# Performance work log

Measured on AMD Instinct MI355X. Metric: run time of the kernel, lower is better.

Reference implementation:

```python
import jax, jax.numpy as jnp
import numpy as np

EPS = 1e-5
DN = ('NCHW', 'OIHW', 'NCHW')


def _bn(x, g, b, m, v):
    # eval-mode batchnorm: per-channel affine with running stats
    scale = (g / jnp.sqrt(v + EPS))[None, :, None, None]
    return (x - m[None, :, None, None]) * scale + b[None, :, None, None]


def setup_inputs() -> dict:
    key = jax.random.key(0)
    ks = jax.random.split(key, 11)
    B, T, Cin, HID, H, W, K = 8, 20, 64, 64, 64, 64, 3
    CC = Cin + HID          # 128 channels into depthwise conv
    C4 = 4 * HID            # 256 gate channels
    return {
        'x': jax.random.normal(ks[0], (B, T, Cin, H, W), jnp.float32),
        'dw_w': jax.random.normal(ks[1], (CC, 1, K, K), jnp.float32) * 0.1,
        'gamma1': jax.random.uniform(ks[2], (CC,), jnp.float32, 0.5, 1.5),
        'beta1': jax.random.normal(ks[3], (CC,), jnp.float32) * 0.1,
        'mean1': jax.random.normal(ks[4], (CC,), jnp.float32) * 0.1,
        'var1': jax.random.uniform(ks[5], (CC,), jnp.float32, 0.5, 1.5),
        'pw_w': jax.random.normal(ks[6], (C4, CC, 1, 1), jnp.float32) * 0.05,
        'gamma2': jax.random.uniform(ks[7], (C4,), jnp.float32, 0.5, 1.5),
        'beta2': jax.random.normal(ks[8], (C4,), jnp.float32) * 0.1,
        'mean2': jax.random.normal(ks[9], (C4,), jnp.float32) * 0.1,
        'var2': jax.random.uniform(ks[10], (C4,), jnp.float32, 0.5, 1.5),
    }


def reference(x, dw_w, gamma1, beta1, mean1, var1, pw_w, gamma2, beta2, mean2, var2):
    B, T, Cin, H, W = x.shape
    hid = pw_w.shape[0] // 4
    cc = dw_w.shape[0]

    def cell(h, c, x_t):
        z = jnp.concatenate([x_t, h], axis=1)                 # (B, Cin+hid, H, W)
        z = jax.lax.conv_general_dilated(z, dw_w, (1, 1), 'SAME',
                                         dimension_numbers=DN,
                                         feature_group_count=cc)
        z = jax.nn.selu(_bn(z, gamma1, beta1, mean1, var1))
        z = jax.lax.conv_general_dilated(z, pw_w, (1, 1), 'SAME',
                                         dimension_numbers=DN)
        z = jax.nn.selu(_bn(z, gamma2, beta2, mean2, var2))   # (B, 4*hid, H, W)
        # NOTE: original code applies Sigmoid to all four gates (incl. g)
        i, f, o, g = jnp.split(jax.nn.sigmoid(z), 4, axis=1)
        c_next = f * c + i * g
        h_next = o * jnp.tanh(c_next)
        return h_next, c_next

    h0 = jnp.zeros((B, hid, H, W), x.dtype)
    c0 = jnp.zeros((B, hid, H, W), x.dtype)

    def step(carry, x_t):
        h, c = cell(carry[0], carry[1], x_t)
        return (h, c), h

    xs = jnp.moveaxis(x, 1, 0)                # (T, B, Cin, H, W)
    _, hs = jax.lax.scan(step, (h0, c0), xs)  # hs: (T, B, hid, H, W)
    return jnp.moveaxis(hs, 0, 1)             # (B, T, hid, H, W)
```

## Files before the change

kernel.cpp:

```cpp
#include <hip/hip_runtime.h>
#include <math.h>

typedef _Float16 half8 __attribute__((ext_vector_type(8)));
typedef float float4v __attribute__((ext_vector_type(4)));

#define SELU_ALPHA 1.6732632423543772f
#define SELU_SCALE 1.0507009873554805f

__device__ __forceinline__ float selu_f(float x) {
    return x > 0.f ? SELU_SCALE * x : SELU_SCALE * SELU_ALPHA * (__expf(x) - 1.f);
}
__device__ __forceinline__ float gate_f(float a, float sc, float sh) {
    float z = a * sc + sh;
    float s = selu_f(z);
    return 1.f / (1.f + __expf(-s));
}

__global__ __launch_bounds__(256) void prep_kernel(
    const float* __restrict__ pw_w,
    const float* __restrict__ g1, const float* __restrict__ b1,
    const float* __restrict__ m1, const float* __restrict__ v1,
    const float* __restrict__ g2, const float* __restrict__ b2,
    const float* __restrict__ m2, const float* __restrict__ v2,
    const float* __restrict__ dw_w,
    _Float16* __restrict__ wB, float* __restrict__ bn2, float* __restrict__ dwpk)
{
    int i = blockIdx.x * 256 + threadIdx.x;
    if (i < 32768) {
        wB[i] = (_Float16)pw_w[i];
    } else if (i < 32768 + 256) {
        int c = i - 32768;
        float sc = g2[c] * rsqrtf(v2[c] + 1e-5f);
        bn2[c] = sc;
        bn2[256 + c] = b2[c] - m2[c] * sc;
    } else if (i < 32768 + 256 + 1536) {
        int j = i - 33024;
        int c = j / 12, k = j - c * 12;
        float val;
        if (k < 9) {
            val = dw_w[c * 9 + k];
        } else {
            float sc = g1[c] * rsqrtf(v1[c] + 1e-5f);
            if (k == 9) val = sc;
            else if (k == 10) val = b1[c] - m1[c] * sc;
            else val = 0.f;
        }
        dwpk[c * 12 + k] = val;
    }
}

__global__ __launch_bounds__(256, 2) void cell_kernel(
    const float* __restrict__ x, const float* __restrict__ hsrc,
    const float* __restrict__ dwpk, const _Float16* __restrict__ wB,
    const float* __restrict__ bn2,
    float* __restrict__ cbuf, float* __restrict__ out, int t)
{
    __shared__ _Float16 Alds[64 * 136];

    int tid = threadIdx.x;
    int bid = blockIdx.y * 64 + blockIdx.x;
    int mapped = (bid & 7) * 64 + (bid >> 3);
    int y0 = mapped & 63;
    int b = mapped >> 6;
    int s0 = y0 << 6;

    int w = tid >> 6;
    int lane = tid & 63;
    int col = lane & 15, quad = lane >> 4;
    int hc = w * 16 + col;

    half8 bfr[4][4];
    #pragma unroll
    for (int nt = 0; nt < 4; ++nt)
        #pragma unroll
        for (int kc = 0; kc < 4; ++kc)
            bfr[nt][kc] = *(const half8*)(wB + (size_t)((nt << 6) + hc) * 128 + kc * 32 + quad * 8);

    bool hwave = (w >= 2);
    const float* src0;
    if (!hwave)
        src0 = x + (((size_t)(b * 20 + t) * 64 + (w << 5)) << 12);
    else
        src0 = hsrc + (((size_t)(b * 20 + (t - 1)) * 64 + ((w - 2) << 5)) << 12);

    if (hwave && t == 0) {
        #pragma unroll
        for (int it = 0; it < 16; ++it) {
            int cc = (w << 5) + (it << 1);
            float sha = dwpk[cc * 12 + 10];
            float shb = dwpk[cc * 12 + 22];
            Alds[lane * 136 + cc]     = (_Float16)selu_f(sha);
            Alds[lane * 136 + cc + 1] = (_Float16)selu_f(shb);
        }
    } else {
        #pragma unroll 4
        for (int it = 0; it < 16; ++it) {
            int cl = it << 1;
            int cc = (w << 5) + cl;
            const float* chA = src0 + ((size_t)cl << 12);
            const float* chB = chA + 4096;
            int p = s0 + lane;
            float a0 = (y0 > 0)  ? chA[p - 64] : 0.f;
            float a1 = chA[p];
            float a2 = (y0 < 63) ? chA[p + 64] : 0.f;
            float c0 = (y0 > 0)  ? chB[p - 64] : 0.f;
            float c1 = chB[p];
            float c2 = (y0 < 63) ? chB[p + 64] : 0.f;
            const float4v* wp = (const float4v*)(dwpk + cc * 12);
            float4v wa0 = wp[0], wa1 = wp[1], wa2 = wp[2];
            float4v wb0 = wp[3], wb1 = wp[4], wb2 = wp[5];
            float P  = fmaf(wa0[0], a0, fmaf(wa0[3], a1, wa1[2] * a2));
            float Q  = fmaf(wa0[1], a0, fmaf(wa1[0], a1, wa1[3] * a2));
            float R  = fmaf(wa0[2], a0, fmaf(wa1[1], a1, wa2[0] * a2));
            float P2 = fmaf(wb0[0], c0, fmaf(wb0[3], c1, wb1[2] * c2));
            float Q2 = fmaf(wb0[1], c0, fmaf(wb1[0], c1, wb1[3] * c2));
            float R2 = fmaf(wb0[2], c0, fmaf(wb1[1], c1, wb2[0] * c2));
            float Pl  = __shfl_up(P, 1);    if (lane == 0)  Pl  = 0.f;
            float Rr  = __shfl_down(R, 1);  if (lane == 63) Rr  = 0.f;
            float P2l = __shfl_up(P2, 1);   if (lane == 0)  P2l = 0.f;
            float R2r = __shfl_down(R2, 1); if (lane == 63) R2r = 0.f;
            float za = fmaf(Pl + Q + Rr,   wa2[1], wa2[2]);
            float zb = fmaf(P2l + Q2 + R2r, wb2[1], wb2[2]);
            Alds[lane * 136 + cc]     = (_Float16)selu_f(za);
            Alds[lane * 136 + cc + 1] = (_Float16)selu_f(zb);
        }
    }

    __syncthreads();

    float4v acc[4][4];
    #pragma unroll
    for (int mt = 0; mt < 4; ++mt)
        #pragma unroll
        for (int nt = 0; nt < 4; ++nt)
            acc[mt][nt] = (float4v){0.f, 0.f, 0.f, 0.f};

    #pragma unroll
    for (int kc = 0; kc < 4; ++kc) {
        half8 a[4];
        #pragma unroll
        for (int mt = 0; mt < 4; ++mt)
            a[mt] = *(const half8*)(Alds + (mt * 16 + col) * 136 + kc * 32 + quad * 8);
        #pragma unroll
        for (int mt = 0; mt < 4; ++mt)
            #pragma unroll
            for (int nt = 0; nt < 4; ++nt)
                acc[mt][nt] = __builtin_amdgcn_mfma_f32_16x16x32_f16(a[mt], bfr[nt][kc], acc[mt][nt], 0, 0, 0);
    }

    float sc[4], sh[4];
    #pragma unroll
    for (int nt = 0; nt < 4; ++nt) {
        sc[nt] = bn2[(nt << 6) + hc];
        sh[nt] = bn2[256 + (nt << 6) + hc];
    }

    size_t cbase = (((size_t)(b * 64 + hc)) << 12) + s0;
    size_t obase = (((size_t)((b * 20 + t) * 64 + hc)) << 12) + s0;

    #pragma unroll
    for (int mt = 0; mt < 4; ++mt) {
        #pragma unroll
        for (int r = 0; r < 4; ++r) {
            int sl = mt * 16 + quad * 4 + r;
            float gi = gate_f(acc[mt][0][r], sc[0], sh[0]);
            float gf = gate_f(acc[mt][1][r], sc[1], sh[1]);
            float go = gate_f(acc[mt][2][r], sc[2], sh[2]);
            float gg = gate_f(acc[mt][3][r], sc[3], sh[3]);
            float cp = (t == 0) ? 0.f : cbuf[cbase + sl];
            float cn = gf * cp + gi * gg;
            cbuf[cbase + sl] = cn;
            float th = 1.f - 2.f / (__expf(2.f * cn) + 1.f);
            out[obase + sl] = go * th;
        }
    }
}

extern "C" void kernel_launch(void* const* d_in, const int* in_sizes, int n_in,
                              void* d_out, int out_size, void* d_ws, size_t ws_size,
                              hipStream_t stream) {
    const float* x    = (const float*)d_in[0];
    const float* dw_w = (const float*)d_in[1];
    const float* g1   = (const float*)d_in[2];
    const float* b1   = (const float*)d_in[3];
    const float* m1   = (const float*)d_in[4];
    const float* v1   = (const float*)d_in[5];
    const float* g2   = (const float*)d_in[6];
    const float* b2   = (const float*)d_in[7];
    const float* m2   = (const float*)d_in[8];
    const float* v2   = (const float*)d_in[9];
    const float* pw_w = (const float*)d_in[6 - 2 + 2];
    (void)pw_w;
    const float* pw_w_ = (const float*)d_in[6];
    const float* g2_   = (const float*)d_in[7];
    const float* b2_   = (const float*)d_in[8];
    const float* m2_   = (const float*)d_in[9];
    const float* v2_   = (const float*)d_in[10];
    float* out = (float*)d_out;

    _Float16* wB16 = (_Float16*)d_ws;
    float* bn2  = (float*)d_ws + 16384;
    float* dwpk = bn2 + 512;
    float* cbuf = dwpk + 1536;

    prep_kernel<<<135, 256, 0, stream>>>(pw_w_, g1, b1, m1, v1,
                                         g2_, b2_, m2_, v2_, dw_w,
                                         wB16, bn2, dwpk);

    for (int t = 0; t < 20; ++t) {
        cell_kernel<<<dim3(64, 8), 256, 0, stream>>>(x, out, dwpk, wB16, bn2,
                                                     cbuf, out, t);
    }
}
```

Baseline: 836.2 us.

## Fuse all timesteps into one persistent kernel with neighbor-row flag sync

Replaces the 20 per-timestep launches with a single persistent kernel of 256 blocks. Each block owns two image rows of one batch element, keeps the cell state in registers instead of a global buffer, and waits on per-row flags set by the neighboring row blocks before reading the previous hidden state for the halo. This removes launch overhead and the global c-state traffic. In exchange it relies on all 256 blocks being co-resident to avoid deadlock, and it adds system-scope fences and spin-waits.

```diff
diff --git a/kernel.cpp b/kernel.cpp
--- a/kernel.cpp
+++ b/kernel.cpp
@@ -23,7 +23,8 @@
     const float* __restrict__ g2, const float* __restrict__ b2,
     const float* __restrict__ m2, const float* __restrict__ v2,
     const float* __restrict__ dw_w,
-    _Float16* __restrict__ wB, float* __restrict__ bn2, float* __restrict__ dwpk)
+    _Float16* __restrict__ wB, float* __restrict__ bn2, float* __restrict__ dwpk,
+    int* __restrict__ flags)
 {
     int i = blockIdx.x * 256 + threadIdx.x;
     if (i < 32768) {
@@ -46,28 +47,70 @@
             else val = 0.f;
         }
         dwpk[c * 12 + k] = val;
-    }
-}
-
-__global__ __launch_bounds__(256, 2) void cell_kernel(
-    const float* __restrict__ x, const float* __restrict__ hsrc,
-    const float* __restrict__ dwpk, const _Float16* __restrict__ wB,
-    const float* __restrict__ bn2,
-    float* __restrict__ cbuf, float* __restrict__ out, int t)
+    } else if (i < 32768 + 256 + 1536 + 256) {
+        flags[i - 34560] = 0;
+    }
+}
+
+__device__ __forceinline__ void dw_rows(
+    const float* __restrict__ src0, const float* __restrict__ dwpk,
+    int ccbase, int y0, int lane, _Float16* Alds)
 {
-    __shared__ _Float16 Alds[64 * 136];
+    int p = (y0 << 6) + lane;
+    #pragma unroll 4
+    for (int it = 0; it < 16; ++it) {
+        int cl = it << 1;
+        int cc = ccbase + cl;
+        const float* chA = src0 + ((size_t)cl << 12);
+        const float* chB = chA + 4096;
+        float a0 = (y0 > 0)  ? chA[p - 64] : 0.f;
+        float a1 = chA[p];
+        float a2 = (y0 < 63) ? chA[p + 64] : 0.f;
+        float c0 = (y0 > 0)  ? chB[p - 64] : 0.f;
+        float c1 = chB[p];
+        float c2 = (y0 < 63) ? chB[p + 64] : 0.f;
+        const float4v* wp = (const float4v*)(dwpk + cc * 12);
+        float4v wa0 = wp[0], wa1 = wp[1], wa2 = wp[2];
+        float4v wb0 = wp[3], wb1 = wp[4], wb2 = wp[5];
+        float P  = fmaf(wa0[0], a0, fmaf(wa0[3], a1, wa1[2] * a2));
+        float Q  = fmaf(wa0[1], a0, fmaf(wa1[0], a1, wa1[3] * a2));
+        float R  = fmaf(wa0[2], a0, fmaf(wa1[1], a1, wa2[0] * a2));
+        float P2 = fmaf(wb0[0], c0, fmaf(wb0[3], c1, wb1[2] * c2));
+        float Q2 = fmaf(wb0[1], c0, fmaf(wb1[0], c1, wb1[3] * c2));
+        float R2 = fmaf(wb0[2], c0, fmaf(wb1[1], c1, wb2[0] * c2));
+        float Pl  = __shfl_up(P, 1);    if (lane == 0)  Pl  = 0.f;
+        float Rr  = __shfl_down(R, 1);  if (lane == 63) Rr  = 0.f;
+        float P2l = __shfl_up(P2, 1);   if (lane == 0)  P2l = 0.f;
+        float R2r = __shfl_down(R2, 1); if (lane == 63) R2r = 0.f;
+        float za = fmaf(Pl + Q + Rr,    wa2[1], wa2[2]);
+        float zb = fmaf(P2l + Q2 + R2r, wb2[1], wb2[2]);
+        Alds[lane * 136 + cc]     = (_Float16)selu_f(za);
+        Alds[lane * 136 + cc + 1] = (_Float16)selu_f(zb);
+    }
+}
+
+__global__ __launch_bounds__(512, 2) void lstm_kernel(
+    const float* __restrict__ x, const float* __restrict__ dwpk,
+    const _Float16* __restrict__ wB, const float* __restrict__ bn2,
+    float* __restrict__ out, int* __restrict__ flags)
+{
+    __shared__ _Float16 Alds[2][64 * 136];
 
     int tid = threadIdx.x;
-    int bid = blockIdx.y * 64 + blockIdx.x;
-    int mapped = (bid & 7) * 64 + (bid >> 3);
-    int y0 = mapped & 63;
-    int b = mapped >> 6;
-    int s0 = y0 << 6;
+    int bid = blockIdx.x;
+    int mapped = (bid & 7) * 32 + (bid >> 3);
+    int ypair = mapped & 31;
+    int b = mapped >> 5;
 
     int w = tid >> 6;
     int lane = tid & 63;
+    int rh = w >> 2;
+    int wq = w & 3;
+    int y0 = (ypair << 1) + rh;
+    int s0 = y0 << 6;
     int col = lane & 15, quad = lane >> 4;
-    int hc = w * 16 + col;
+    int hc = wq * 16 + col;
+    bool hwave = (wq >= 2);
 
     half8 bfr[4][4];
     #pragma unroll
@@ -75,78 +118,6 @@
         #pragma unroll
         for (int kc = 0; kc < 4; ++kc)
             bfr[nt][kc] = *(const half8*)(wB + (size_t)((nt << 6) + hc) * 128 + kc * 32 + quad * 8);
-
-    bool hwave = (w >= 2);
-    const float* src0;
-    if (!hwave)
-        src0 = x + (((size_t)(b * 20 + t) * 64 + (w << 5)) << 12);
-    else
-        src0 = hsrc + (((size_t)(b * 20 + (t - 1)) * 64 + ((w - 2) << 5)) << 12);
-
-    if (hwave && t == 0) {
-        #pragma unroll
-        for (int it = 0; it < 16; ++it) {
-            int cc = (w << 5) + (it << 1);
-            float sha = dwpk[cc * 12 + 10];
-            float shb = dwpk[cc * 12 + 22];
-            Alds[lane * 136 + cc]     = (_Float16)selu_f(sha);
-            Alds[lane * 136 + cc + 1] = (_Float16)selu_f(shb);
-        }
-    } else {
-        #pragma unroll 4
-        for (int it = 0; it < 16; ++it) {
-            int cl = it << 1;
-            int cc = (w << 5) + cl;
-            const float* chA = src0 + ((size_t)cl << 12);
-            const float* chB = chA + 4096;
-            int p = s0 + lane;
-            float a0 = (y0 > 0)  ? chA[p - 64] : 0.f;
-            float a1 = chA[p];
-            float a2 = (y0 < 63) ? chA[p + 64] : 0.f;
-            float c0 = (y0 > 0)  ? chB[p - 64] : 0.f;
-            float c1 = chB[p];
-            float c2 = (y0 < 63) ? chB[p + 64] : 0.f;
-            const float4v* wp = (const float4v*)(dwpk + cc * 12);
-            float4v wa0 = wp[0], wa1 = wp[1], wa2 = wp[2];
-            float4v wb0 = wp[3], wb1 = wp[4], wb2 = wp[5];
-            float P  = fmaf(wa0[0], a0, fmaf(wa0[3], a1, wa1[2] * a2));
-            float Q  = fmaf(wa0[1], a0, fmaf(wa1[0], a1, wa1[3] * a2));
-            float R  = fmaf(wa0[2], a0, fmaf(wa1[1], a1, wa2[0] * a2));
-            float P2 = fmaf(wb0[0], c0, fmaf(wb0[3], c1, wb1[2] * c2));
-            float Q2 = fmaf(wb0[1], c0, fmaf(wb1[0], c1, wb1[3] * c2));
-            float R2 = fmaf(wb0[2], c0, fmaf(wb1[1], c1, wb2[0] * c2));
-            float Pl  = __shfl_up(P, 1);    if (lane == 0)  Pl  = 0.f;
-            float Rr  = __shfl_down(R, 1);  if (lane == 63) Rr  = 0.f;
-            float P2l = __shfl_up(P2, 1);   if (lane == 0)  P2l = 0.f;
-            float R2r = __shfl_down(R2, 1); if (lane == 63) R2r = 0.f;
-            float za = fmaf(Pl + Q + Rr,   wa2[1], wa2[2]);
-            float zb = fmaf(P2l + Q2 + R2r, wb2[1], wb2[2]);
-            Alds[lane * 136 + cc]     = (_Float16)selu_f(za);
-            Alds[lane * 136 + cc + 1] = (_Float16)selu_f(zb);
-        }
-    }
-
-    __syncthreads();
-
-    float4v acc[4][4];
-    #pragma unroll
-    for (int mt = 0; mt < 4; ++mt)
-        #pragma unroll
-        for (int nt = 0; nt < 4; ++nt)
-            acc[mt][nt] = (float4v){0.f, 0.f, 0.f, 0.f};
-
-    #pragma unroll
-    for (int kc = 0; kc < 4; ++kc) {
-        half8 a[4];
-        #pragma unroll
-        for (int mt = 0; mt < 4; ++mt)
-            a[mt] = *(const half8*)(Alds + (mt * 16 + col) * 136 + kc * 32 + quad * 8);
-        #pragma unroll
-        for (int mt = 0; mt < 4; ++mt)
-            #pragma unroll
-            for (int nt = 0; nt < 4; ++nt)
-                acc[mt][nt] = __builtin_amdgcn_mfma_f32_16x16x32_f16(a[mt], bfr[nt][kc], acc[mt][nt], 0, 0, 0);
-    }
 
     float sc[4], sh[4];
     #pragma unroll
@@ -155,23 +126,83 @@
         sh[nt] = bn2[256 + (nt << 6) + hc];
     }
 
-    size_t cbase = (((size_t)(b * 64 + hc)) << 12) + s0;
-    size_t obase = (((size_t)((b * 20 + t) * 64 + hc)) << 12) + s0;
-
+    float creg[4][4];
     #pragma unroll
-    for (int mt = 0; mt < 4; ++mt) {
-        #pragma unroll
-        for (int r = 0; r < 4; ++r) {
-            int sl = mt * 16 + quad * 4 + r;
-            float gi = gate_f(acc[mt][0][r], sc[0], sh[0]);
-            float gf = gate_f(acc[mt][1][r], sc[1], sh[1]);
-            float go = gate_f(acc[mt][2][r], sc[2], sh[2]);
-            float gg = gate_f(acc[mt][3][r], sc[3], sh[3]);
-            float cp = (t == 0) ? 0.f : cbuf[cbase + sl];
-            float cn = gf * cp + gi * gg;
-            cbuf[cbase + sl] = cn;
-            float th = 1.f - 2.f / (__expf(2.f * cn) + 1.f);
-            out[obase + sl] = go * th;
+    for (int mt = 0; mt < 4; ++mt)
+        #pragma unroll
+        for (int r = 0; r < 4; ++r) creg[mt][r] = 0.f;
+
+    int* myflags = flags + (b << 5);
+    _Float16* A = Alds[rh];
+
+    for (int t = 0; t < 20; ++t) {
+        if (!hwave) {
+            const float* src0 = x + ((((size_t)(b * 20 + t)) * 64 + (wq << 5)) << 12);
+            dw_rows(src0, dwpk, wq << 5, y0, lane, A);
+        } else if (t == 0) {
+            #pragma unroll
+            for (int it = 0; it < 16; ++it) {
+                int cc = (wq << 5) + (it << 1);
+                float sha = dwpk[cc * 12 + 10];
+                float shb = dwpk[cc * 12 + 22];
+                A[lane * 136 + cc]     = (_Float16)selu_f(sha);
+                A[lane * 136 + cc + 1] = (_Float16)selu_f(shb);
+            }
+        } else {
+            int nb = (rh == 0) ? (ypair - 1) : (ypair + 1);
+            if (nb >= 0 && nb < 32) {
+                while (__hip_atomic_load(&myflags[nb], __ATOMIC_ACQUIRE,
+                                         __HIP_MEMORY_SCOPE_SYSTEM) < t)
+                    __builtin_amdgcn_s_sleep(2);
+            }
+            const float* src0 = out + ((((size_t)(b * 20 + (t - 1))) * 64 + ((wq - 2) << 5)) << 12);
+            dw_rows(src0, dwpk, wq << 5, y0, lane, A);
+        }
+
+        __syncthreads();
+
+        float4v acc[4][4];
+        #pragma unroll
+        for (int mt = 0; mt < 4; ++mt)
+            #pragma unroll
+            for (int nt = 0; nt < 4; ++nt)
+                acc[mt][nt] = (float4v){0.f, 0.f, 0.f, 0.f};
+
+        #pragma unroll
+        for (int kc = 0; kc < 4; ++kc) {
+            half8 a[4];
+            #pragma unroll
+            for (int mt = 0; mt < 4; ++mt)
+                a[mt] = *(const half8*)(A + (mt * 16 + col) * 136 + kc * 32 + quad * 8);
+            #pragma unroll
+            for (int mt = 0; mt < 4; ++mt)
+                #pragma unroll
+                for (int nt = 0; nt < 4; ++nt)
+                    acc[mt][nt] = __builtin_amdgcn_mfma_f32_16x16x32_f16(a[mt], bfr[nt][kc], acc[mt][nt], 0, 0, 0);
+        }
+
+        size_t obase = (((size_t)((b * 20 + t) * 64 + hc)) << 12) + s0;
+        #pragma unroll
+        for (int mt = 0; mt < 4; ++mt) {
+            #pragma unroll
+            for (int r = 0; r < 4; ++r) {
+                int sl = mt * 16 + quad * 4 + r;
+                float gi = gate_f(acc[mt][0][r], sc[0], sh[0]);
+                float gf = gate_f(acc[mt][1][r], sc[1], sh[1]);
+                float go = gate_f(acc[mt][2][r], sc[2], sh[2]);
+                float gg = gate_f(acc[mt][3][r], sc[3], sh[3]);
+                float cn = gf * creg[mt][r] + gi * gg;
+                creg[mt][r] = cn;
+                float th = 1.f - 2.f / (__expf(2.f * cn) + 1.f);
+                out[obase + sl] = go * th;
+            }
+        }
+
+        __syncthreads();
+        if (tid == 0) {
+            __threadfence_system();
+            __hip_atomic_store(&myflags[ypair], t + 1, __ATOMIC_RELEASE,
+                               __HIP_MEMORY_SCOPE_SYSTEM);
         }
     }
 }
@@ -185,30 +216,21 @@
     const float* b1   = (const float*)d_in[3];
     const float* m1   = (const float*)d_in[4];
     const float* v1   = (const float*)d_in[5];
-    const float* g2   = (const float*)d_in[6];
-    const float* b2   = (const float*)d_in[7];
-    const float* m2   = (const float*)d_in[8];
-    const float* v2   = (const float*)d_in[9];
-    const float* pw_w = (const float*)d_in[6 - 2 + 2];
-    (void)pw_w;
-    const float* pw_w_ = (const float*)d_in[6];
-    const float* g2_   = (const float*)d_in[7];
-    const float* b2_   = (const float*)d_in[8];
-    const float* m2_   = (const float*)d_in[9];
-    const float* v2_   = (const float*)d_in[10];
+    const float* pw_w = (const float*)d_in[6];
+    const float* g2   = (const float*)d_in[7];
+    const float* b2   = (const float*)d_in[8];
+    const float* m2   = (const float*)d_in[9];
+    const float* v2   = (const float*)d_in[10];
     float* out = (float*)d_out;
 
     _Float16* wB16 = (_Float16*)d_ws;
     float* bn2  = (float*)d_ws + 16384;
     float* dwpk = bn2 + 512;
-    float* cbuf = dwpk + 1536;
-
-    prep_kernel<<<135, 256, 0, stream>>>(pw_w_, g1, b1, m1, v1,
-                                         g2_, b2_, m2_, v2_, dw_w,
-                                         wB16, bn2, dwpk);
-
-    for (int t = 0; t < 20; ++t) {
-        cell_kernel<<<dim3(64, 8), 256, 0, stream>>>(x, out, dwpk, wB16, bn2,
-                                                     cbuf, out, t);
-    }
-}
+    int* flags  = (int*)(dwpk + 1536);
+
+    prep_kernel<<<136, 256, 0, stream>>>(pw_w, g1, b1, m1, v1,
+                                         g2, b2, m2, v2, dw_w,
+                                         wB16, bn2, dwpk, flags);
+
+    lstm_kernel<<<256, 512, 0, stream>>>(x, dwpk, wB16, bn2, out, flags);
+}
```

New measurement: 1.141 ms. +36.5%, slower.

## Precompute x-path depthwise conv for all timesteps; widen cell kernel to 512 threads

Applied to the files above, without the earlier changes.

Moves the depthwise conv, BN and SELU for the input half of the channels out of the recurrent loop into one batched kernel over all timesteps. It writes fp16 activations in a pixel-major layout that the per-step kernel copies straight into LDS. The cell kernel now uses 512 threads, with 8 waves splitting the h-channel depthwise work and the two row halves of the MFMA tile, which aims at more parallelism per step. In exchange it adds an extra fp16 workspace buffer that is written and read back, and relies on the workspace being large enough.

```diff
diff --git a/kernel.cpp b/kernel.cpp
--- a/kernel.cpp
+++ b/kernel.cpp
@@ -14,6 +14,34 @@
     float z = a * sc + sh;
     float s = selu_f(z);
     return 1.f / (1.f + __expf(-s));
+}
+
+__device__ __forceinline__ void dw2(
+    const float* __restrict__ chA, const float* __restrict__ chB,
+    const float* __restrict__ wbase, int y0, int p, int lane,
+    float& za, float& zb)
+{
+    float a0 = (y0 > 0)  ? chA[p - 64] : 0.f;
+    float a1 = chA[p];
+    float a2 = (y0 < 63) ? chA[p + 64] : 0.f;
+    float c0 = (y0 > 0)  ? chB[p - 64] : 0.f;
+    float c1 = chB[p];
+    float c2 = (y0 < 63) ? chB[p + 64] : 0.f;
+    const float4v* wp = (const float4v*)wbase;
+    float4v wa0 = wp[0], wa1 = wp[1], wa2 = wp[2];
+    float4v wb0 = wp[3], wb1 = wp[4], wb2 = wp[5];
+    float P  = fmaf(wa0[0], a0, fmaf(wa0[3], a1, wa1[2] * a2));
+    float Q  = fmaf(wa0[1], a0, fmaf(wa1[0], a1, wa1[3] * a2));
+    float R  = fmaf(wa0[2], a0, fmaf(wa1[1], a1, wa2[0] * a2));
+    float P2 = fmaf(wb0[0], c0, fmaf(wb0[3], c1, wb1[2] * c2));
+    float Q2 = fmaf(wb0[1], c0, fmaf(wb1[0], c1, wb1[3] * c2));
+    float R2 = fmaf(wb0[2], c0, fmaf(wb1[1], c1, wb2[0] * c2));
+    float Pl  = __shfl_up(P, 1);    if (lane == 0)  Pl  = 0.f;
+    float Rr  = __shfl_down(R, 1);  if (lane == 63) Rr  = 0.f;
+    float P2l = __shfl_up(P2, 1);   if (lane == 0)  P2l = 0.f;
+    float R2r = __shfl_down(R2, 1); if (lane == 63) R2r = 0.f;
+    za = fmaf(Pl + Q + Rr,    wa2[1], wa2[2]);
+    zb = fmaf(P2l + Q2 + R2r, wb2[1], wb2[2]);
 }
 
 __global__ __launch_bounds__(256) void prep_kernel(
@@ -49,25 +77,52 @@
     }
 }
 
-__global__ __launch_bounds__(256, 2) void cell_kernel(
-    const float* __restrict__ x, const float* __restrict__ hsrc,
+__global__ __launch_bounds__(256) void zx_kernel(
+    const float* __restrict__ x, const float* __restrict__ dwpk,
+    _Float16* __restrict__ z1x)
+{
+    int tid = threadIdx.x;
+    int y0 = blockIdx.x, t = blockIdx.y, b = blockIdx.z;
+    int w = tid >> 6, lane = tid & 63;
+    const float* src0 = x + (((size_t)(b * 20 + t) * 64 + (w << 4)) << 12);
+    int p = (y0 << 6) + lane;
+    half8 r[2];
+    #pragma unroll
+    for (int it = 0; it < 8; ++it) {
+        int cl = it << 1;
+        int cc = (w << 4) + cl;
+        const float* chA = src0 + ((size_t)cl << 12);
+        const float* chB = chA + 4096;
+        float za, zb;
+        dw2(chA, chB, dwpk + cc * 12, y0, p, lane, za, zb);
+        r[cl >> 3][cl & 7]       = (_Float16)selu_f(za);
+        r[cl >> 3][(cl & 7) + 1] = (_Float16)selu_f(zb);
+    }
+    size_t o = ((((size_t)(b * 20 + t) * 64 + y0) * 64 + lane) << 6) + (w << 4);
+    *(half8*)(z1x + o)     = r[0];
+    *(half8*)(z1x + o + 8) = r[1];
+}
+
+__global__ __launch_bounds__(512, 4) void cell_kernel(
+    const _Float16* __restrict__ z1x, const float* __restrict__ hsrc,
     const float* __restrict__ dwpk, const _Float16* __restrict__ wB,
     const float* __restrict__ bn2,
     float* __restrict__ cbuf, float* __restrict__ out, int t)
 {
-    __shared__ _Float16 Alds[64 * 136];
+    __shared__ _Float16 A[64 * 136];
 
     int tid = threadIdx.x;
-    int bid = blockIdx.y * 64 + blockIdx.x;
+    int bid = blockIdx.x;
     int mapped = (bid & 7) * 64 + (bid >> 3);
     int y0 = mapped & 63;
     int b = mapped >> 6;
     int s0 = y0 << 6;
 
-    int w = tid >> 6;
-    int lane = tid & 63;
+    int w = tid >> 6, lane = tid & 63;
     int col = lane & 15, quad = lane >> 4;
-    int hc = w * 16 + col;
+    int rhalf = w >> 2;
+    int wq = w & 3;
+    int hc = (wq << 4) + col;
 
     half8 bfr[4][4];
     #pragma unroll
@@ -75,78 +130,6 @@
         #pragma unroll
         for (int kc = 0; kc < 4; ++kc)
             bfr[nt][kc] = *(const half8*)(wB + (size_t)((nt << 6) + hc) * 128 + kc * 32 + quad * 8);
-
-    bool hwave = (w >= 2);
-    const float* src0;
-    if (!hwave)
-        src0 = x + (((size_t)(b * 20 + t) * 64 + (w << 5)) << 12);
-    else
-        src0 = hsrc + (((size_t)(b * 20 + (t - 1)) * 64 + ((w - 2) << 5)) << 12);
-
-    if (hwave && t == 0) {
-        #pragma unroll
-        for (int it = 0; it < 16; ++it) {
-            int cc = (w << 5) + (it << 1);
-            float sha = dwpk[cc * 12 + 10];
-            float shb = dwpk[cc * 12 + 22];
-            Alds[lane * 136 + cc]     = (_Float16)selu_f(sha);
-            Alds[lane * 136 + cc + 1] = (_Float16)selu_f(shb);
-        }
-    } else {
-        #pragma unroll 4
-        for (int it = 0; it < 16; ++it) {
-            int cl = it << 1;
-            int cc = (w << 5) + cl;
-            const float* chA = src0 + ((size_t)cl << 12);
-            const float* chB = chA + 4096;
-            int p = s0 + lane;
-            float a0 = (y0 > 0)  ? chA[p - 64] : 0.f;
-            float a1 = chA[p];
-            float a2 = (y0 < 63) ? chA[p + 64] : 0.f;
-            float c0 = (y0 > 0)  ? chB[p - 64] : 0.f;
-            float c1 = chB[p];
-            float c2 = (y0 < 63) ? chB[p + 64] : 0.f;
-            const float4v* wp = (const float4v*)(dwpk + cc * 12);
-            float4v wa0 = wp[0], wa1 = wp[1], wa2 = wp[2];
-            float4v wb0 = wp[3], wb1 = wp[4], wb2 = wp[5];
-            float P  = fmaf(wa0[0], a0, fmaf(wa0[3], a1, wa1[2] * a2));
-            float Q  = fmaf(wa0[1], a0, fmaf(wa1[0], a1, wa1[3] * a2));
-            float R  = fmaf(wa0[2], a0, fmaf(wa1[1], a1, wa2[0] * a2));
-            float P2 = fmaf(wb0[0], c0, fmaf(wb0[3], c1, wb1[2] * c2));
-            float Q2 = fmaf(wb0[1], c0, fmaf(wb1[0], c1, wb1[3] * c2));
-            float R2 = fmaf(wb0[2], c0, fmaf(wb1[1], c1, wb2[0] * c2));
-            float Pl  = __shfl_up(P, 1);    if (lane == 0)  Pl  = 0.f;
-            float Rr  = __shfl_down(R, 1);  if (lane == 63) Rr  = 0.f;
-            float P2l = __shfl_up(P2, 1);   if (lane == 0)  P2l = 0.f;
-            float R2r = __shfl_down(R2, 1); if (lane == 63) R2r = 0.f;
-            float za = fmaf(Pl + Q + Rr,   wa2[1], wa2[2]);
-            float zb = fmaf(P2l + Q2 + R2r, wb2[1], wb2[2]);
-            Alds[lane * 136 + cc]     = (_Float16)selu_f(za);
-            Alds[lane * 136 + cc + 1] = (_Float16)selu_f(zb);
-        }
-    }
-
-    __syncthreads();
-
-    float4v acc[4][4];
-    #pragma unroll
-    for (int mt = 0; mt < 4; ++mt)
-        #pragma unroll
-        for (int nt = 0; nt < 4; ++nt)
-            acc[mt][nt] = (float4v){0.f, 0.f, 0.f, 0.f};
-
-    #pragma unroll
-    for (int kc = 0; kc < 4; ++kc) {
-        half8 a[4];
-        #pragma unroll
-        for (int mt = 0; mt < 4; ++mt)
-            a[mt] = *(const half8*)(Alds + (mt * 16 + col) * 136 + kc * 32 + quad * 8);
-        #pragma unroll
-        for (int mt = 0; mt < 4; ++mt)
-            #pragma unroll
-            for (int nt = 0; nt < 4; ++nt)
-                acc[mt][nt] = __builtin_amdgcn_mfma_f32_16x16x32_f16(a[mt], bfr[nt][kc], acc[mt][nt], 0, 0, 0);
-    }
 
     float sc[4], sh[4];
     #pragma unroll
@@ -155,14 +138,68 @@
         sh[nt] = bn2[256 + (nt << 6) + hc];
     }
 
+    {
+        int px = tid >> 3, part = tid & 7;
+        const half8 v = *(const half8*)(z1x +
+            ((((size_t)(b * 20 + t) * 64 + y0) * 64 + px) << 6) + (part << 3));
+        *(half8*)(A + px * 136 + (part << 3)) = v;
+    }
+
+    if (t == 0) {
+        #pragma unroll
+        for (int it = 0; it < 4; ++it) {
+            int cc = 64 + (w << 3) + (it << 1);
+            A[lane * 136 + cc]     = (_Float16)selu_f(dwpk[cc * 12 + 10]);
+            A[lane * 136 + cc + 1] = (_Float16)selu_f(dwpk[cc * 12 + 22]);
+        }
+    } else {
+        const float* src0 = hsrc + (((size_t)(b * 20 + (t - 1)) * 64 + (w << 3)) << 12);
+        int p = s0 + lane;
+        #pragma unroll
+        for (int it = 0; it < 4; ++it) {
+            int cl = it << 1;
+            int cc = 64 + (w << 3) + cl;
+            const float* chA = src0 + ((size_t)cl << 12);
+            const float* chB = chA + 4096;
+            float za, zb;
+            dw2(chA, chB, dwpk + cc * 12, y0, p, lane, za, zb);
+            A[lane * 136 + cc]     = (_Float16)selu_f(za);
+            A[lane * 136 + cc + 1] = (_Float16)selu_f(zb);
+        }
+    }
+
+    __syncthreads();
+
+    float4v acc[2][4];
+    #pragma unroll
+    for (int mt = 0; mt < 2; ++mt)
+        #pragma unroll
+        for (int nt = 0; nt < 4; ++nt)
+            acc[mt][nt] = (float4v){0.f, 0.f, 0.f, 0.f};
+
+    #pragma unroll
+    for (int kc = 0; kc < 4; ++kc) {
+        half8 a[2];
+        #pragma unroll
+        for (int mt = 0; mt < 2; ++mt)
+            a[mt] = *(const half8*)(A + ((rhalf << 5) + (mt << 4) + col) * 136
+                                      + (kc << 5) + (quad << 3));
+        #pragma unroll
+        for (int mt = 0; mt < 2; ++mt)
+            #pragma unroll
+            for (int nt = 0; nt < 4; ++nt)
+                acc[mt][nt] = __builtin_amdgcn_mfma_f32_16x16x32_f16(
+                    a[mt], bfr[nt][kc], acc[mt][nt], 0, 0, 0);
+    }
+
     size_t cbase = (((size_t)(b * 64 + hc)) << 12) + s0;
     size_t obase = (((size_t)((b * 20 + t) * 64 + hc)) << 12) + s0;
 
     #pragma unroll
-    for (int mt = 0; mt < 4; ++mt) {
+    for (int mt = 0; mt < 2; ++mt) {
         #pragma unroll
         for (int r = 0; r < 4; ++r) {
-            int sl = mt * 16 + quad * 4 + r;
+            int sl = (rhalf << 5) + (mt << 4) + (quad << 2) + r;
             float gi = gate_f(acc[mt][0][r], sc[0], sh[0]);
             float gf = gate_f(acc[mt][1][r], sc[1], sh[1]);
             float go = gate_f(acc[mt][2][r], sc[2], sh[2]);
@@ -185,30 +222,27 @@
     const float* b1   = (const float*)d_in[3];
     const float* m1   = (const float*)d_in[4];
     const float* v1   = (const float*)d_in[5];
-    const float* g2   = (const float*)d_in[6];
-    const float* b2   = (const float*)d_in[7];
-    const float* m2   = (const float*)d_in[8];
-    const float* v2   = (const float*)d_in[9];
-    const float* pw_w = (const float*)d_in[6 - 2 + 2];
-    (void)pw_w;
-    const float* pw_w_ = (const float*)d_in[6];
-    const float* g2_   = (const float*)d_in[7];
-    const float* b2_   = (const float*)d_in[8];
-    const float* m2_   = (const float*)d_in[9];
-    const float* v2_   = (const float*)d_in[10];
+    const float* pw_w = (const float*)d_in[6];
+    const float* g2   = (const float*)d_in[7];
+    const float* b2   = (const float*)d_in[8];
+    const float* m2   = (const float*)d_in[9];
+    const float* v2   = (const float*)d_in[10];
     float* out = (float*)d_out;
 
     _Float16* wB16 = (_Float16*)d_ws;
     float* bn2  = (float*)d_ws + 16384;
     float* dwpk = bn2 + 512;
     float* cbuf = dwpk + 1536;
-
-    prep_kernel<<<135, 256, 0, stream>>>(pw_w_, g1, b1, m1, v1,
-                                         g2_, b2_, m2_, v2_, dw_w,
+    _Float16* z1x = (_Float16*)(cbuf + (size_t)8 * 64 * 4096);
+
+    prep_kernel<<<135, 256, 0, stream>>>(pw_w, g1, b1, m1, v1,
+                                         g2, b2, m2, v2, dw_w,
                                          wB16, bn2, dwpk);
 
+    zx_kernel<<<dim3(64, 20, 8), 256, 0, stream>>>(x, dwpk, z1x);
+
     for (int t = 0; t < 20; ++t) {
-        cell_kernel<<<dim3(64, 8), 256, 0, stream>>>(x, out, dwpk, wB16, bn2,
-                                                     cbuf, out, t);
-    }
-}
+        cell_kernel<<<512, 512, 0, stream>>>(z1x, out, dwpk, wB16, bn2,
+                                             cbuf, out, t);
+    }
+}
```

Result: slower. 875.5 us (+4.7%).
